# Kernel optimization log

Measured on AMD Instinct MI355X. Metric: run time of the kernel, lower is better.

Reference implementation:

```python
import jax, jax.numpy as jnp
import numpy as np

N, D = 8192, 4096

def setup_inputs() -> dict:
    key = jax.random.key(0)
    kX, = jax.random.split(key, 1)
    X = jax.random.normal(kX, (N, D), dtype=jnp.float32)
    mean = jnp.zeros((D,), dtype=jnp.float32)
    df = jnp.ones((1,), dtype=jnp.float32)
    return {"X": X, "mean": mean, "df": df}

def reference(X, mean, df):
    # Original torch code: diag(log(1 + (X-mean)@(X-mean).T / df)).
    # diag((X-m)(X-m)^T) == rowwise sum of squared differences, and
    # diag(log(M)) == log(diag(M)) for elementwise log, so this is exact.
    d = X.shape[-1]
    diff = X - mean                      # [N, d]
    sq = jnp.sum(diff * diff, axis=-1)   # [N] = diag of the NxN outer product
    logden = jnp.log(1.0 + sq / df[0])   # [N]
    unden = 0.5 * (df[0] + d) * logden   # [N]
    return -unden
```

## Files before the change

kernel.cpp:

```cpp
#include <hip/hip_runtime.h>
#include <math.h>


#define ROWS 8192
#define COLS 4096

__global__ __launch_bounds__(256) void
row_logden_kernel(const float* __restrict__ X,
                  const float* __restrict__ mean,
                  const float* __restrict__ df,
                  float* __restrict__ out) {
    const int row = blockIdx.x;
    const int t = threadIdx.x;

    const float4* __restrict__ xr =
        reinterpret_cast<const float4*>(X + (size_t)row * COLS);
    const float4* __restrict__ mr =
        reinterpret_cast<const float4*>(mean);

    float acc = 0.0f;
#pragma unroll
    for (int k = 0; k < 4; ++k) {
        const int i = t + k * 256;
        const float4 x = xr[i];
        const float4 m = mr[i];
        const float dx = x.x - m.x;
        const float dy = x.y - m.y;
        const float dz = x.z - m.z;
        const float dw = x.w - m.w;
        acc += dx * dx + dy * dy + dz * dz + dw * dw;
    }

#pragma unroll
    for (int off = 32; off > 0; off >>= 1)
        acc += __shfl_down(acc, off, 64);

    __shared__ float partial[4];
    const int wave = t >> 6;
    const int lane = t & 63;
    if (lane == 0) partial[wave] = acc;
    __syncthreads();

    if (t == 0) {
        const float s = partial[0] + partial[1] + partial[2] + partial[3];
        const float dfv = df[0];
        out[row] = -0.5f * (dfv + (float)COLS) * logf(1.0f + s / dfv);
    }
}

extern "C" void kernel_launch(void* const* d_in, const int* in_sizes, int n_in,
                              void* d_out, int out_size, void* d_ws, size_t ws_size,
                              hipStream_t stream) {
    const float* X    = (const float*)d_in[0];
    const float* mean = (const float*)d_in[1];
    const float* df   = (const float*)d_in[2];
    float* out = (float*)d_out;

    row_logden_kernel<<<ROWS, 256, 0, stream>>>(X, mean, df, out);
}
```

Before: 186.3 us.

## Assign one row per wavefront and use nontemporal loads for X

```diff
diff --git a/kernel.cpp b/kernel.cpp
--- a/kernel.cpp
+++ b/kernel.cpp
@@ -5,46 +5,39 @@
 #define ROWS 8192
 #define COLS 4096
 
-__global__ __launch_bounds__(256) void
+typedef float f32x4 __attribute__((ext_vector_type(4)));
+
+__global__ __launch_bounds__(256, 4) void
 row_logden_kernel(const float* __restrict__ X,
                   const float* __restrict__ mean,
                   const float* __restrict__ df,
                   float* __restrict__ out) {
-    const int row = blockIdx.x;
-    const int t = threadIdx.x;
+    const int wave = threadIdx.x >> 6;
+    const int lane = threadIdx.x & 63;
+    const int row  = blockIdx.x * 4 + wave;
 
-    const float4* __restrict__ xr =
-        reinterpret_cast<const float4*>(X + (size_t)row * COLS);
-    const float4* __restrict__ mr =
-        reinterpret_cast<const float4*>(mean);
+    const f32x4* __restrict__ xr =
+        reinterpret_cast<const f32x4*>(X + (size_t)row * COLS);
+    const f32x4* __restrict__ mr =
+        reinterpret_cast<const f32x4*>(mean);
 
     float acc = 0.0f;
 #pragma unroll
-    for (int k = 0; k < 4; ++k) {
-        const int i = t + k * 256;
-        const float4 x = xr[i];
-        const float4 m = mr[i];
-        const float dx = x.x - m.x;
-        const float dy = x.y - m.y;
-        const float dz = x.z - m.z;
-        const float dw = x.w - m.w;
-        acc += dx * dx + dy * dy + dz * dz + dw * dw;
+    for (int k = 0; k < 16; ++k) {
+        const int i = lane + k * 64;
+        const f32x4 x = __builtin_nontemporal_load(&xr[i]);
+        const f32x4 m = mr[i];
+        const f32x4 d = x - m;
+        acc += d.x * d.x + d.y * d.y + d.z * d.z + d.w * d.w;
     }
 
 #pragma unroll
     for (int off = 32; off > 0; off >>= 1)
         acc += __shfl_down(acc, off, 64);
 
-    __shared__ float partial[4];
-    const int wave = t >> 6;
-    const int lane = t & 63;
-    if (lane == 0) partial[wave] = acc;
-    __syncthreads();
-
-    if (t == 0) {
-        const float s = partial[0] + partial[1] + partial[2] + partial[3];
+    if (lane == 0) {
         const float dfv = df[0];
-        out[row] = -0.5f * (dfv + (float)COLS) * logf(1.0f + s / dfv);
+        out[row] = -0.5f * (dfv + (float)COLS) * logf(1.0f + acc / dfv);
     }
 }
 
@@ -56,5 +49,5 @@
     const float* df   = (const float*)d_in[2];
     float* out = (float*)d_out;
 
-    row_logden_kernel<<<ROWS, 256, 0, stream>>>(X, mean, df, out);
+    row_logden_kernel<<<ROWS / 4, 256, 0, stream>>>(X, mean, df, out);
 }
```

New measurement: 179.0 us. 1.04x faster.
